# Kernel optimization log

Measured on AMD Instinct MI355X. Metric: run time of the kernel, lower is better.

The kernel has to match this reference:

```python
import jax, jax.numpy as jnp
import numpy as np

B, T, IN, H, L = 256, 80, 39, 256, 5


def _xavier(key, shape):
    fan_out, fan_in = shape[0], shape[1]
    std = (2.0 / (fan_in + fan_out)) ** 0.5
    return std * jax.random.normal(key, shape, dtype=jnp.float32)


def setup_inputs() -> dict:
    key = jax.random.key(0)
    ks = jax.random.split(key, 4 + 2 * L)
    x = jax.random.normal(ks[0], (B, T, IN), dtype=jnp.float32)
    # PyTorch LSTM params, gate order (i, f, g, o); biases zero per init.
    W_ih0 = _xavier(ks[1], (4 * H, IN))                       # layer 0 input weights
    W_ih_rest = jnp.stack([_xavier(ks[2 + l], (4 * H, H)) for l in range(L - 1)])  # [L-1,4H,H]
    W_hh = jnp.stack([_xavier(ks[1 + L + l], (4 * H, H)) for l in range(L)])       # [L,4H,H]
    b_ih = jnp.zeros((L, 4 * H), dtype=jnp.float32)
    b_hh = jnp.zeros((L, 4 * H), dtype=jnp.float32)
    fc_w = _xavier(ks[2 * L + 1], (1, H))
    fc_b = jnp.zeros((1,), dtype=jnp.float32)
    return {"x": x, "W_ih0": W_ih0, "W_ih_rest": W_ih_rest, "W_hh": W_hh,
            "b_ih": b_ih, "b_hh": b_hh, "fc_w": fc_w, "fc_b": fc_b}


def _lstm_layer(xs, W_ih, W_hh_l, b_ih_l, b_hh_l):
    # xs: [B,T,D]. Precompute input projection for all timesteps (one big GEMM).
    x_proj = jnp.einsum('btd,gd->btg', xs, W_ih) + b_ih_l + b_hh_l  # [B,T,4H]

    def step(carry, xp):
        h, c = carry
        gates = xp + h @ W_hh_l.T                 # [B,4H]
        i, f, g, o = jnp.split(gates, 4, axis=-1)
        c = jax.nn.sigmoid(f) * c + jax.nn.sigmoid(i) * jnp.tanh(g)
        h = jax.nn.sigmoid(o) * jnp.tanh(c)
        return (h, c), h

    b = xs.shape[0]
    h0 = jnp.zeros((b, H), dtype=xs.dtype)
    _, hs = jax.lax.scan(step, (h0, h0), jnp.swapaxes(x_proj, 0, 1))
    return jnp.swapaxes(hs, 0, 1)  # [B,T,H]


def reference(x, W_ih0, W_ih_rest, W_hh, b_ih, b_hh, fc_w, fc_b):
    h = _lstm_layer(x, W_ih0, W_hh[0], b_ih[0], b_hh[0])
    for l in range(1, L):
        h = _lstm_layer(h, W_ih_rest[l - 1], W_hh[l], b_ih[l], b_hh[l])
    out = jnp.einsum('bth,oh->bto', h, fc_w) + fc_b  # [B,T,1]
    return out[..., 0]  # [B,T]
```

## Files before the change

kernel.cpp:

```cpp
#include <hip/hip_runtime.h>

#define B_ 256
#define T_ 80
#define IN_ 39
#define H_ 256
#define G_ 1024
#define L_ 5
#define TC_ 16
#define NCH_ 5

#define XP_FLOATS   (B_ * TC_ * G_)
#define HBUF_FLOATS (B_ * T_ * H_)
#define CBUF_FLOATS (B_ * H_)
#define WG_FLOATS   (L_ * G_ * H_)
#define HX_FLOATS   (2 * 32 * 2048)
#define FLG_OFF_FLOATS (XP_FLOATS + HBUF_FLOATS + CBUF_FLOATS + WG_FLOATS + HX_FLOATS)

#define AG __HIP_MEMORY_SCOPE_AGENT

__device__ __forceinline__ float sigm(float x) { return 1.0f / (1.0f + expf(-x)); }
__device__ __forceinline__ void fma4(float4& a, float s, const float4& w) {
    a.x = fmaf(s, w.x, a.x); a.y = fmaf(s, w.y, a.y);
    a.z = fmaf(s, w.z, a.z); a.w = fmaf(s, w.w, a.w);
}
__device__ __forceinline__ void red4(float4& a) {
    a.x += __shfl_xor(a.x, 32); a.y += __shfl_xor(a.y, 32);
    a.z += __shfl_xor(a.z, 32); a.w += __shfl_xor(a.w, 32);
}
__device__ __forceinline__ float lo32(unsigned long long v) { return __uint_as_float((unsigned)v); }
__device__ __forceinline__ float hi32(unsigned long long v) { return __uint_as_float((unsigned)(v >> 32)); }

extern "C" __global__ void __launch_bounds__(256)
wt_kernel(const float* __restrict__ Whh, float* __restrict__ Wg) {
    const int gid = blockIdx.x * 256 + threadIdx.x;
    const int g4 = gid & 3;
    const int j  = (gid >> 2) & 31;
    const int k  = (gid >> 7) & 255;
    const int s  = (gid >> 15) & 7;
    const int l  = gid >> 18;
    Wg[gid] = Whh[((size_t)(l * 1024 + g4 * 256 + s * 32 + j)) * 256 + k];
}

extern "C" __global__ void __launch_bounds__(256)
proj_kernel(const float* __restrict__ src, const float* __restrict__ Wih,
            const float* __restrict__ bihl, const float* __restrict__ bhhl,
            float* __restrict__ xp, int K, int t0) {
    __shared__ float As[16 * 68];
    __shared__ float Bs[16 * 68];
    const int tid = threadIdx.x;
    const int mt = blockIdx.x >> 4, nt = blockIdx.x & 15;
    const int tx = tid & 15, ty = tid >> 4;
    const int lr = tid >> 2, lc4 = (tid & 3) << 2;

    const int ar = mt * 64 + lr;
    const int ab = ar >> 4;
    const int at = t0 + (ar & 15);
    const float* arow = src + ((size_t)ab * T_ + at) * K;
    const float* brow = Wih + (size_t)(nt * 64 + lr) * K;

    float acc[4][4];
    #pragma unroll
    for (int i = 0; i < 4; ++i)
        #pragma unroll
        for (int j = 0; j < 4; ++j) acc[i][j] = 0.0f;

    for (int k0 = 0; k0 < K; k0 += 16) {
        __syncthreads();
        if (K == IN_) {
            #pragma unroll
            for (int i = 0; i < 4; ++i) {
                int k = k0 + lc4 + i;
                As[(lc4 + i) * 68 + lr] = (k < IN_) ? arow[k] : 0.0f;
                Bs[(lc4 + i) * 68 + lr] = (k < IN_) ? brow[k] : 0.0f;
            }
        } else {
            float4 av = *(const float4*)(arow + k0 + lc4);
            float4 bv = *(const float4*)(brow + k0 + lc4);
            As[(lc4 + 0) * 68 + lr] = av.x;
            As[(lc4 + 1) * 68 + lr] = av.y;
            As[(lc4 + 2) * 68 + lr] = av.z;
            As[(lc4 + 3) * 68 + lr] = av.w;
            Bs[(lc4 + 0) * 68 + lr] = bv.x;
            Bs[(lc4 + 1) * 68 + lr] = bv.y;
            Bs[(lc4 + 2) * 68 + lr] = bv.z;
            Bs[(lc4 + 3) * 68 + lr] = bv.w;
        }
        __syncthreads();
        #pragma unroll
        for (int kk = 0; kk < 16; ++kk) {
            float4 a4 = *(const float4*)&As[kk * 68 + ty * 4];
            float4 b4 = *(const float4*)&Bs[kk * 68 + tx * 4];
            acc[0][0] += a4.x * b4.x; acc[0][1] += a4.x * b4.y;
            acc[0][2] += a4.x * b4.z; acc[0][3] += a4.x * b4.w;
            acc[1][0] += a4.y * b4.x; acc[1][1] += a4.y * b4.y;
            acc[1][2] += a4.y * b4.z; acc[1][3] += a4.y * b4.w;
            acc[2][0] += a4.z * b4.x; acc[2][1] += a4.z * b4.y;
            acc[2][2] += a4.z * b4.z; acc[2][3] += a4.z * b4.w;
            acc[3][0] += a4.w * b4.x; acc[3][1] += a4.w * b4.y;
            acc[3][2] += a4.w * b4.z; acc[3][3] += a4.w * b4.w;
        }
    }
    const int col = nt * 64 + tx * 4;
    const float bs0 = bihl[col + 0] + bhhl[col + 0];
    const float bs1 = bihl[col + 1] + bhhl[col + 1];
    const float bs2 = bihl[col + 2] + bhhl[col + 2];
    const float bs3 = bihl[col + 3] + bhhl[col + 3];
    #pragma unroll
    for (int i = 0; i < 4; ++i) {
        const int row = mt * 64 + ty * 4 + i;
        float4 o;
        o.x = acc[i][0] + bs0; o.y = acc[i][1] + bs1;
        o.z = acc[i][2] + bs2; o.w = acc[i][3] + bs3;
        *(float4*)&xp[(size_t)row * G_ + col] = o;
    }
}

extern "C" __global__ void __launch_bounds__(512, 2)
rec5_kernel(const float* __restrict__ xp, const float* __restrict__ Wg_l,
            float* __restrict__ hbuf, float* __restrict__ cbuf,
            float* __restrict__ hx, int* __restrict__ flg,
            int t0, int chkb, int first) {
    __shared__ float sH[2048];
    __shared__ float sP[8 * 32 * 36];

    const int tid = threadIdx.x;
    const int bid = blockIdx.x;
    const int grp = bid & 31;
    const int s   = bid >> 5;
    const int jj  = tid & 31;
    const int ks  = tid >> 5;
    const int w   = tid >> 6;
    const int fb  = (tid >> 5) & 7;
    const int fj  = tid & 31;
    const int bglob = grp * 8 + fb;
    const int unit  = s * 32 + fj;
    int* flg_g = flg + grp * 32;

    const float4* Wg4 = (const float4*)Wg_l + (size_t)s * 8192;
    float4 wreg[16];
    #pragma unroll
    for (int kk = 0; kk < 16; ++kk)
        wreg[kk] = Wg4[(size_t)(ks * 16 + kk) * 32 + jj];

    float creg = 0.0f;
    if (tid < 256 && !first) creg = cbuf[(size_t)bglob * H_ + unit];

    const float4* sH4 = (const float4*)sH;

    for (int tt = 0; tt < TC_; ++tt) {
        const int t = t0 + tt;

        float x0 = 0.f, x1 = 0.f, x2 = 0.f, x3 = 0.f;
        if (tid < 256) {
            const size_t xrow = ((size_t)bglob * TC_ + tt) * G_ + unit;
            x0 = xp[xrow];
            x1 = xp[xrow + 256];
            x2 = xp[xrow + 512];
            x3 = xp[xrow + 768];
        }

        if (tt == 0) {
            if (first) {
                for (int i = tid; i < 2048; i += 512) sH[i] = 0.0f;
            } else if (tid < 256) {
                const int u = tid;
                #pragma unroll
                for (int bb = 0; bb < 8; ++bb)
                    sH[u * 8 + bb] = hbuf[((size_t)(grp * 8 + bb) * T_ + (t0 - 1)) * H_ + u];
            }
        } else {
            if (tid < 8) {
                const int tgt = chkb + tt;
                while (__hip_atomic_load(flg_g + tid, __ATOMIC_RELAXED, AG) < tgt)
                    __builtin_amdgcn_s_sleep(1);
            }
            __syncthreads();
            if (tid < 256) {
                const unsigned long long* hs =
                    (const unsigned long long*)(hx + (size_t)(((tt - 1) & 1) * 32 + grp) * 2048);
                const int u = tid;
                unsigned long long v0 = __hip_atomic_load(hs + u * 4 + 0, __ATOMIC_RELAXED, AG);
                unsigned long long v1 = __hip_atomic_load(hs + u * 4 + 1, __ATOMIC_RELAXED, AG);
                unsigned long long v2 = __hip_atomic_load(hs + u * 4 + 2, __ATOMIC_RELAXED, AG);
                unsigned long long v3 = __hip_atomic_load(hs + u * 4 + 3, __ATOMIC_RELAXED, AG);
                float4 fa, fbv;
                fa.x = lo32(v0); fa.y = hi32(v0); fa.z = lo32(v1); fa.w = hi32(v1);
                fbv.x = lo32(v2); fbv.y = hi32(v2); fbv.z = lo32(v3); fbv.w = hi32(v3);
                *(float4*)&sH[u * 8] = fa;
                *(float4*)&sH[u * 8 + 4] = fbv;
            }
        }

        __syncthreads();

        float4 a0 = {0,0,0,0}, a1 = {0,0,0,0}, a2 = {0,0,0,0}, a3 = {0,0,0,0};
        float4 a4 = {0,0,0,0}, a5 = {0,0,0,0}, a6 = {0,0,0,0}, a7 = {0,0,0,0};
        #pragma unroll
        for (int kk = 0; kk < 16; ++kk) {
            const int k = ks * 16 + kk;
            const float4 wv = wreg[kk];
            const float4 ha = sH4[k * 2];
            const float4 hb = sH4[k * 2 + 1];
            fma4(a0, ha.x, wv); fma4(a1, ha.y, wv);
            fma4(a2, ha.z, wv); fma4(a3, ha.w, wv);
            fma4(a4, hb.x, wv); fma4(a5, hb.y, wv);
            fma4(a6, hb.z, wv); fma4(a7, hb.w, wv);
        }
        red4(a0); red4(a1); red4(a2); red4(a3);
        red4(a4); red4(a5); red4(a6); red4(a7);
        if ((tid & 63) < 32) {
            float4* pp = (float4*)&sP[(w * 32 + jj) * 36];
            pp[0] = a0; pp[1] = a1; pp[2] = a2; pp[3] = a3;
            pp[4] = a4; pp[5] = a5; pp[6] = a6; pp[7] = a7;
        }
        __syncthreads();

        if (tid < 256) {
            float4 g4;
            g4.x = x0; g4.y = x1; g4.z = x2; g4.w = x3;
            #pragma unroll
            for (int w2 = 0; w2 < 8; ++w2) {
                const float4 pw = *(const float4*)&sP[(w2 * 32 + fj) * 36 + fb * 4];
                g4.x += pw.x; g4.y += pw.y; g4.z += pw.z; g4.w += pw.w;
            }
            const float I = sigm(g4.x);
            const float F = sigm(g4.y);
            const float Gt = tanhf(g4.z);
            const float O = sigm(g4.w);
            creg = F * creg + I * Gt;
            const float hval = O * tanhf(creg);
            hbuf[((size_t)bglob * T_ + t) * H_ + unit] = hval;

            if (tt < TC_ - 1) {
                __hip_atomic_store(hx + (size_t)((tt & 1) * 32 + grp) * 2048 + unit * 8 + fb,
                                   hval, __ATOMIC_RELAXED, AG);
            }
        }

        if (tt < TC_ - 1) {
            asm volatile("s_waitcnt vmcnt(0)" ::: "memory");
            __syncthreads();
            if (tid == 0)
                __hip_atomic_store(flg_g + s, chkb + tt + 1, __ATOMIC_RELAXED, AG);
        }
    }

    if (tid < 256) cbuf[(size_t)bglob * H_ + unit] = creg;
}

extern "C" __global__ void __launch_bounds__(128)
fc_kernel(const float* __restrict__ hbuf, const float* __restrict__ fcw,
          const float* __restrict__ fcb, float* __restrict__ out) {
    __shared__ float wsm[256];
    const int tid = threadIdx.x;
    const int b = blockIdx.x;
    if (tid < 64) ((float4*)wsm)[tid] = ((const float4*)fcw)[tid];
    __syncthreads();
    if (tid < T_) {
        const float4* h4p = (const float4*)(hbuf + ((size_t)b * T_ + tid) * H_);
        const float4* w4p = (const float4*)wsm;
        float acc = fcb[0];
        #pragma unroll 8
        for (int k4 = 0; k4 < 64; ++k4) {
            float4 h4 = h4p[k4], w4 = w4p[k4];
            acc += h4.x * w4.x + h4.y * w4.y + h4.z * w4.z + h4.w * w4.w;
        }
        out[b * T_ + tid] = acc;
    }
}

extern "C" void kernel_launch(void* const* d_in, const int* in_sizes, int n_in,
                              void* d_out, int out_size, void* d_ws, size_t ws_size,
                              hipStream_t stream) {
    (void)in_sizes; (void)n_in; (void)out_size; (void)ws_size;
    const float* x    = (const float*)d_in[0];
    const float* Wih0 = (const float*)d_in[1];
    const float* Wihr = (const float*)d_in[2];
    const float* Whh  = (const float*)d_in[3];
    const float* bih  = (const float*)d_in[4];
    const float* bhh  = (const float*)d_in[5];
    const float* fcw  = (const float*)d_in[6];
    const float* fcb  = (const float*)d_in[7];
    float* out = (float*)d_out;
    float* ws  = (float*)d_ws;

    float* xp   = ws;
    float* hbuf = ws + XP_FLOATS;
    float* cbuf = hbuf + HBUF_FLOATS;
    float* wg   = cbuf + CBUF_FLOATS;
    float* hx   = wg + WG_FLOATS;
    int*   flg  = (int*)(ws + FLG_OFF_FLOATS);

    hipMemsetAsync(flg, 0, 32 * 32 * sizeof(int), stream);
    hipLaunchKernelGGL(wt_kernel, dim3(WG_FLOATS / 256), dim3(256), 0, stream, Whh, wg);

    for (int l = 0; l < L_; ++l) {
        const int K = (l == 0) ? IN_ : H_;
        const float* src = (l == 0) ? x : hbuf;
        const float* Wih = (l == 0) ? Wih0 : (Wihr + (size_t)(l - 1) * G_ * H_);
        const float* Wg_l = wg + (size_t)l * (G_ * H_);
        for (int ch = 0; ch < NCH_; ++ch) {
            const int t0 = ch * TC_;
            const int chkb = (l * NCH_ + ch) * (TC_ - 1);
            hipLaunchKernelGGL(proj_kernel, dim3(1024), dim3(256), 0, stream,
                               src, Wih, bih + l * G_, bhh + l * G_, xp, K, t0);
            hipLaunchKernelGGL(rec5_kernel, dim3(256), dim3(512), 0, stream,
                               xp, Wg_l, hbuf, cbuf, hx, flg, t0, chkb, ch == 0 ? 1 : 0);
        }
    }
    hipLaunchKernelGGL(fc_kernel, dim3(B_), dim3(128), 0, stream, hbuf, fcw, fcb, out);
}
```

Before: 2.582 ms.

## Overlap next-chunk input projection with current recurrence via helper blocks

Merges the per-chunk projection GEMM into the recurrent kernel. An extra 256 helper blocks compute the input projection for the next (layer, chunk) into a double-buffered xp, while the first 256 blocks run the current chunk's recurrence. Only the first projection is launched on its own, so the serial projection launch between recurrence chunks goes away and the GEMM hides behind the latency-bound recurrence. The cost is a second xp buffer and helper blocks sharing CUs with the spin-waiting recurrence blocks, which may slow the critical path.

```diff
diff --git a/kernel.cpp b/kernel.cpp
--- a/kernel.cpp
+++ b/kernel.cpp
@@ -14,7 +14,6 @@
 #define CBUF_FLOATS (B_ * H_)
 #define WG_FLOATS   (L_ * G_ * H_)
 #define HX_FLOATS   (2 * 32 * 2048)
-#define FLG_OFF_FLOATS (XP_FLOATS + HBUF_FLOATS + CBUF_FLOATS + WG_FLOATS + HX_FLOATS)
 
 #define AG __HIP_MEMORY_SCOPE_AGENT
 
@@ -116,136 +115,217 @@
 }
 
 extern "C" __global__ void __launch_bounds__(512, 2)
-rec5_kernel(const float* __restrict__ xp, const float* __restrict__ Wg_l,
-            float* __restrict__ hbuf, float* __restrict__ cbuf,
-            float* __restrict__ hx, int* __restrict__ flg,
-            int t0, int chkb, int first) {
-    __shared__ float sH[2048];
-    __shared__ float sP[8 * 32 * 36];
+fused_kernel(const float* __restrict__ xp, const float* __restrict__ Wg_l,
+             float* __restrict__ hbuf, float* __restrict__ cbuf,
+             float* __restrict__ hx, int* __restrict__ flg,
+             int t0, int chkb, int first,
+             int do_help, float* __restrict__ xpn, const float* __restrict__ hsrc,
+             const float* __restrict__ wih_n, const float* __restrict__ bih_n,
+             const float* __restrict__ bhh_n, int Kn, int t0n) {
+    __shared__ float smem[11264];
 
     const int tid = threadIdx.x;
     const int bid = blockIdx.x;
-    const int grp = bid & 31;
-    const int s   = bid >> 5;
-    const int jj  = tid & 31;
-    const int ks  = tid >> 5;
-    const int w   = tid >> 6;
-    const int fb  = (tid >> 5) & 7;
-    const int fj  = tid & 31;
-    const int bglob = grp * 8 + fb;
-    const int unit  = s * 32 + fj;
-    int* flg_g = flg + grp * 32;
-
-    const float4* Wg4 = (const float4*)Wg_l + (size_t)s * 8192;
-    float4 wreg[16];
-    #pragma unroll
-    for (int kk = 0; kk < 16; ++kk)
-        wreg[kk] = Wg4[(size_t)(ks * 16 + kk) * 32 + jj];
-
-    float creg = 0.0f;
-    if (tid < 256 && !first) creg = cbuf[(size_t)bglob * H_ + unit];
-
-    const float4* sH4 = (const float4*)sH;
-
-    for (int tt = 0; tt < TC_; ++tt) {
-        const int t = t0 + tt;
-
-        float x0 = 0.f, x1 = 0.f, x2 = 0.f, x3 = 0.f;
-        if (tid < 256) {
-            const size_t xrow = ((size_t)bglob * TC_ + tt) * G_ + unit;
-            x0 = xp[xrow];
-            x1 = xp[xrow + 256];
-            x2 = xp[xrow + 512];
-            x3 = xp[xrow + 768];
+
+    if (bid < 256) {
+        float* sH = smem;
+        float* sP = smem + 2048;
+        const int grp = bid & 31;
+        const int s   = bid >> 5;
+        const int jj  = tid & 31;
+        const int ks  = tid >> 5;
+        const int w   = tid >> 6;
+        const int fb  = (tid >> 5) & 7;
+        const int fj  = tid & 31;
+        const int bglob = grp * 8 + fb;
+        const int unit  = s * 32 + fj;
+        int* flg_g = flg + grp * 32;
+
+        const float4* Wg4 = (const float4*)Wg_l + (size_t)s * 8192;
+        float4 wreg[16];
+        #pragma unroll
+        for (int kk = 0; kk < 16; ++kk)
+            wreg[kk] = Wg4[(size_t)(ks * 16 + kk) * 32 + jj];
+
+        float creg = 0.0f;
+        if (tid < 256 && !first) creg = cbuf[(size_t)bglob * H_ + unit];
+
+        const float4* sH4 = (const float4*)sH;
+
+        for (int tt = 0; tt < TC_; ++tt) {
+            const int t = t0 + tt;
+
+            float x0 = 0.f, x1 = 0.f, x2 = 0.f, x3 = 0.f;
+            if (tid < 256) {
+                const size_t xrow = ((size_t)bglob * TC_ + tt) * G_ + unit;
+                x0 = xp[xrow];
+                x1 = xp[xrow + 256];
+                x2 = xp[xrow + 512];
+                x3 = xp[xrow + 768];
+            }
+
+            if (tt == 0) {
+                if (first) {
+                    for (int i = tid; i < 2048; i += 512) sH[i] = 0.0f;
+                } else if (tid < 256) {
+                    const int u = tid;
+                    #pragma unroll
+                    for (int bb = 0; bb < 8; ++bb)
+                        sH[u * 8 + bb] = hbuf[((size_t)(grp * 8 + bb) * T_ + (t0 - 1)) * H_ + u];
+                }
+            } else {
+                if (tid < 8) {
+                    const int tgt = chkb + tt;
+                    while (__hip_atomic_load(flg_g + tid, __ATOMIC_RELAXED, AG) < tgt)
+                        __builtin_amdgcn_s_sleep(1);
+                }
+                __syncthreads();
+                if (tid < 256) {
+                    const unsigned long long* hs =
+                        (const unsigned long long*)(hx + (size_t)(((tt - 1) & 1) * 32 + grp) * 2048);
+                    const int u = tid;
+                    unsigned long long v0 = __hip_atomic_load(hs + u * 4 + 0, __ATOMIC_RELAXED, AG);
+                    unsigned long long v1 = __hip_atomic_load(hs + u * 4 + 1, __ATOMIC_RELAXED, AG);
+                    unsigned long long v2 = __hip_atomic_load(hs + u * 4 + 2, __ATOMIC_RELAXED, AG);
+                    unsigned long long v3 = __hip_atomic_load(hs + u * 4 + 3, __ATOMIC_RELAXED, AG);
+                    float4 fa, fbv;
+                    fa.x = lo32(v0); fa.y = hi32(v0); fa.z = lo32(v1); fa.w = hi32(v1);
+                    fbv.x = lo32(v2); fbv.y = hi32(v2); fbv.z = lo32(v3); fbv.w = hi32(v3);
+                    *(float4*)&sH[u * 8] = fa;
+                    *(float4*)&sH[u * 8 + 4] = fbv;
+                }
+            }
+
+            __syncthreads();
+
+            float4 a0 = {0,0,0,0}, a1 = {0,0,0,0}, a2 = {0,0,0,0}, a3 = {0,0,0,0};
+            float4 a4 = {0,0,0,0}, a5 = {0,0,0,0}, a6 = {0,0,0,0}, a7 = {0,0,0,0};
+            #pragma unroll
+            for (int kk = 0; kk < 16; ++kk) {
+                const int k = ks * 16 + kk;
+                const float4 wv = wreg[kk];
+                const float4 ha = sH4[k * 2];
+                const float4 hb = sH4[k * 2 + 1];
+                fma4(a0, ha.x, wv); fma4(a1, ha.y, wv);
+                fma4(a2, ha.z, wv); fma4(a3, ha.w, wv);
+                fma4(a4, hb.x, wv); fma4(a5, hb.y, wv);
+                fma4(a6, hb.z, wv); fma4(a7, hb.w, wv);
+            }
+            red4(a0); red4(a1); red4(a2); red4(a3);
+            red4(a4); red4(a5); red4(a6); red4(a7);
+            if ((tid & 63) < 32) {
+                float4* pp = (float4*)&sP[(w * 32 + jj) * 36];
+                pp[0] = a0; pp[1] = a1; pp[2] = a2; pp[3] = a3;
+                pp[4] = a4; pp[5] = a5; pp[6] = a6; pp[7] = a7;
+            }
+            __syncthreads();
+
+            if (tid < 256) {
+                float4 g4;
+                g4.x = x0; g4.y = x1; g4.z = x2; g4.w = x3;
+                #pragma unroll
+                for (int w2 = 0; w2 < 8; ++w2) {
+                    const float4 pw = *(const float4*)&sP[(w2 * 32 + fj) * 36 + fb * 4];
+                    g4.x += pw.x; g4.y += pw.y; g4.z += pw.z; g4.w += pw.w;
+                }
+                const float I = sigm(g4.x);
+                const float F = sigm(g4.y);
+                const float Gt = tanhf(g4.z);
+                const float O = sigm(g4.w);
+                creg = F * creg + I * Gt;
+                const float hval = O * tanhf(creg);
+                hbuf[((size_t)bglob * T_ + t) * H_ + unit] = hval;
+                if (tt < TC_ - 1) {
+                    __hip_atomic_store(hx + (size_t)((tt & 1) * 32 + grp) * 2048 + unit * 8 + fb,
+                                       hval, __ATOMIC_RELAXED, AG);
+                }
+            }
+
+            if (tt < TC_ - 1) {
+                asm volatile("s_waitcnt vmcnt(0)" ::: "memory");
+                __syncthreads();
+                if (tid == 0)
+                    __hip_atomic_store(flg_g + s, chkb + tt + 1, __ATOMIC_RELAXED, AG);
+            }
         }
 
-        if (tt == 0) {
-            if (first) {
-                for (int i = tid; i < 2048; i += 512) sH[i] = 0.0f;
-            } else if (tid < 256) {
-                const int u = tid;
+        if (tid < 256) cbuf[(size_t)bglob * H_ + unit] = creg;
+    } else {
+        if (!do_help) return;
+        const int hb = bid - 256;
+        const int team = tid >> 8;
+        const int t2 = tid & 255;
+        float* As = smem + team * 2176;
+        float* Bs = As + 1088;
+        const int tx = t2 & 15, ty = t2 >> 4;
+        const int lr = t2 >> 2, lc4 = (t2 & 3) << 2;
+
+        for (int r = 0; r < 2; ++r) {
+            const int tile = hb * 4 + team * 2 + r;
+            const int mt = tile >> 4, nt = tile & 15;
+            const int ar = mt * 64 + lr;
+            const int ab = ar >> 4;
+            const int at = t0n + (ar & 15);
+            const float* arow = hsrc + ((size_t)ab * T_ + at) * Kn;
+            const float* brow = wih_n + (size_t)(nt * 64 + lr) * Kn;
+
+            float acc[4][4];
+            #pragma unroll
+            for (int i = 0; i < 4; ++i)
                 #pragma unroll
-                for (int bb = 0; bb < 8; ++bb)
-                    sH[u * 8 + bb] = hbuf[((size_t)(grp * 8 + bb) * T_ + (t0 - 1)) * H_ + u];
-            }
-        } else {
-            if (tid < 8) {
-                const int tgt = chkb + tt;
-                while (__hip_atomic_load(flg_g + tid, __ATOMIC_RELAXED, AG) < tgt)
-                    __builtin_amdgcn_s_sleep(1);
-            }
-            __syncthreads();
-            if (tid < 256) {
-                const unsigned long long* hs =
-                    (const unsigned long long*)(hx + (size_t)(((tt - 1) & 1) * 32 + grp) * 2048);
-                const int u = tid;
-                unsigned long long v0 = __hip_atomic_load(hs + u * 4 + 0, __ATOMIC_RELAXED, AG);
-                unsigned long long v1 = __hip_atomic_load(hs + u * 4 + 1, __ATOMIC_RELAXED, AG);
-                unsigned long long v2 = __hip_atomic_load(hs + u * 4 + 2, __ATOMIC_RELAXED, AG);
-                unsigned long long v3 = __hip_atomic_load(hs + u * 4 + 3, __ATOMIC_RELAXED, AG);
-                float4 fa, fbv;
-                fa.x = lo32(v0); fa.y = hi32(v0); fa.z = lo32(v1); fa.w = hi32(v1);
-                fbv.x = lo32(v2); fbv.y = hi32(v2); fbv.z = lo32(v3); fbv.w = hi32(v3);
-                *(float4*)&sH[u * 8] = fa;
-                *(float4*)&sH[u * 8 + 4] = fbv;
-            }
-        }
-
-        __syncthreads();
-
-        float4 a0 = {0,0,0,0}, a1 = {0,0,0,0}, a2 = {0,0,0,0}, a3 = {0,0,0,0};
-        float4 a4 = {0,0,0,0}, a5 = {0,0,0,0}, a6 = {0,0,0,0}, a7 = {0,0,0,0};
-        #pragma unroll
-        for (int kk = 0; kk < 16; ++kk) {
-            const int k = ks * 16 + kk;
-            const float4 wv = wreg[kk];
-            const float4 ha = sH4[k * 2];
-            const float4 hb = sH4[k * 2 + 1];
-            fma4(a0, ha.x, wv); fma4(a1, ha.y, wv);
-            fma4(a2, ha.z, wv); fma4(a3, ha.w, wv);
-            fma4(a4, hb.x, wv); fma4(a5, hb.y, wv);
-            fma4(a6, hb.z, wv); fma4(a7, hb.w, wv);
-        }
-        red4(a0); red4(a1); red4(a2); red4(a3);
-        red4(a4); red4(a5); red4(a6); red4(a7);
-        if ((tid & 63) < 32) {
-            float4* pp = (float4*)&sP[(w * 32 + jj) * 36];
-            pp[0] = a0; pp[1] = a1; pp[2] = a2; pp[3] = a3;
-            pp[4] = a4; pp[5] = a5; pp[6] = a6; pp[7] = a7;
-        }
-        __syncthreads();
-
-        if (tid < 256) {
-            float4 g4;
-            g4.x = x0; g4.y = x1; g4.z = x2; g4.w = x3;
+                for (int j = 0; j < 4; ++j) acc[i][j] = 0.0f;
+
+            for (int k0 = 0; k0 < Kn; k0 += 16) {
+                __syncthreads();
+                if (Kn == IN_) {
+                    #pragma unroll
+                    for (int i = 0; i < 4; ++i) {
+                        int k = k0 + lc4 + i;
+                        As[(lc4 + i) * 68 + lr] = (k < IN_) ? arow[k] : 0.0f;
+                        Bs[(lc4 + i) * 68 + lr] = (k < IN_) ? brow[k] : 0.0f;
+                    }
+                } else {
+                    float4 av = *(const float4*)(arow + k0 + lc4);
+                    float4 bv = *(const float4*)(brow + k0 + lc4);
+                    As[(lc4 + 0) * 68 + lr] = av.x;
+                    As[(lc4 + 1) * 68 + lr] = av.y;
+                    As[(lc4 + 2) * 68 + lr] = av.z;
+                    As[(lc4 + 3) * 68 + lr] = av.w;
+                    Bs[(lc4 + 0) * 68 + lr] = bv.x;
+                    Bs[(lc4 + 1) * 68 + lr] = bv.y;
+                    Bs[(lc4 + 2) * 68 + lr] = bv.z;
+                    Bs[(lc4 + 3) * 68 + lr] = bv.w;
+                }
+                __syncthreads();
+                #pragma unroll
+                for (int kk = 0; kk < 16; ++kk) {
+                    float4 a4 = *(const float4*)&As[kk * 68 + ty * 4];
+                    float4 b4 = *(const float4*)&Bs[kk * 68 + tx * 4];
+                    acc[0][0] += a4.x * b4.x; acc[0][1] += a4.x * b4.y;
+                    acc[0][2] += a4.x * b4.z; acc[0][3] += a4.x * b4.w;
+                    acc[1][0] += a4.y * b4.x; acc[1][1] += a4.y * b4.y;
+                    acc[1][2] += a4.y * b4.z; acc[1][3] += a4.y * b4.w;
+                    acc[2][0] += a4.z * b4.x; acc[2][1] += a4.z * b4.y;
+                    acc[2][2] += a4.z * b4.z; acc[2][3] += a4.z * b4.w;
+                    acc[3][0] += a4.w * b4.x; acc[3][1] += a4.w * b4.y;
+                    acc[3][2] += a4.w * b4.z; acc[3][3] += a4.w * b4.w;
+                }
+            }
+            const int col = nt * 64 + tx * 4;
+            const float bs0 = bih_n[col + 0] + bhh_n[col + 0];
+            const float bs1 = bih_n[col + 1] + bhh_n[col + 1];
+            const float bs2 = bih_n[col + 2] + bhh_n[col + 2];
+            const float bs3 = bih_n[col + 3] + bhh_n[col + 3];
             #pragma unroll
-            for (int w2 = 0; w2 < 8; ++w2) {
-                const float4 pw = *(const float4*)&sP[(w2 * 32 + fj) * 36 + fb * 4];
-                g4.x += pw.x; g4.y += pw.y; g4.z += pw.z; g4.w += pw.w;
-            }
-            const float I = sigm(g4.x);
-            const float F = sigm(g4.y);
-            const float Gt = tanhf(g4.z);
-            const float O = sigm(g4.w);
-            creg = F * creg + I * Gt;
-            const float hval = O * tanhf(creg);
-            hbuf[((size_t)bglob * T_ + t) * H_ + unit] = hval;
-
-            if (tt < TC_ - 1) {
-                __hip_atomic_store(hx + (size_t)((tt & 1) * 32 + grp) * 2048 + unit * 8 + fb,
-                                   hval, __ATOMIC_RELAXED, AG);
-            }
-        }
-
-        if (tt < TC_ - 1) {
-            asm volatile("s_waitcnt vmcnt(0)" ::: "memory");
-            __syncthreads();
-            if (tid == 0)
-                __hip_atomic_store(flg_g + s, chkb + tt + 1, __ATOMIC_RELAXED, AG);
+            for (int i = 0; i < 4; ++i) {
+                const int row = mt * 64 + ty * 4 + i;
+                float4 o;
+                o.x = acc[i][0] + bs0; o.y = acc[i][1] + bs1;
+                o.z = acc[i][2] + bs2; o.w = acc[i][3] + bs3;
+                *(float4*)&xpn[(size_t)row * G_ + col] = o;
+            }
         }
     }
-
-    if (tid < 256) cbuf[(size_t)bglob * H_ + unit] = creg;
 }
 
 extern "C" __global__ void __launch_bounds__(128)
@@ -284,29 +364,40 @@
     float* out = (float*)d_out;
     float* ws  = (float*)d_ws;
 
-    float* xp   = ws;
-    float* hbuf = ws + XP_FLOATS;
+    float* xp0  = ws;
+    float* xp1  = ws + XP_FLOATS;
+    float* hbuf = ws + 2 * XP_FLOATS;
     float* cbuf = hbuf + HBUF_FLOATS;
     float* wg   = cbuf + CBUF_FLOATS;
     float* hx   = wg + WG_FLOATS;
-    int*   flg  = (int*)(ws + FLG_OFF_FLOATS);
+    int*   flg  = (int*)(hx + HX_FLOATS);
 
     hipMemsetAsync(flg, 0, 32 * 32 * sizeof(int), stream);
     hipLaunchKernelGGL(wt_kernel, dim3(WG_FLOATS / 256), dim3(256), 0, stream, Whh, wg);
-
-    for (int l = 0; l < L_; ++l) {
-        const int K = (l == 0) ? IN_ : H_;
-        const float* src = (l == 0) ? x : hbuf;
-        const float* Wih = (l == 0) ? Wih0 : (Wihr + (size_t)(l - 1) * G_ * H_);
+    hipLaunchKernelGGL(proj_kernel, dim3(1024), dim3(256), 0, stream,
+                       x, Wih0, bih, bhh, xp0, IN_, 0);
+
+    for (int q = 0; q < L_ * NCH_; ++q) {
+        const int l = q / NCH_, ch = q % NCH_;
+        float* xpc = (q & 1) ? xp1 : xp0;
         const float* Wg_l = wg + (size_t)l * (G_ * H_);
-        for (int ch = 0; ch < NCH_; ++ch) {
-            const int t0 = ch * TC_;
-            const int chkb = (l * NCH_ + ch) * (TC_ - 1);
-            hipLaunchKernelGGL(proj_kernel, dim3(1024), dim3(256), 0, stream,
-                               src, Wih, bih + l * G_, bhh + l * G_, xp, K, t0);
-            hipLaunchKernelGGL(rec5_kernel, dim3(256), dim3(512), 0, stream,
-                               xp, Wg_l, hbuf, cbuf, hx, flg, t0, chkb, ch == 0 ? 1 : 0);
-        }
+        const int t0 = ch * TC_;
+        const int chkb = q * (TC_ - 1);
+        const int first = (ch == 0) ? 1 : 0;
+
+        const int do_help = (q < L_ * NCH_ - 1) ? 1 : 0;
+        const int q2 = do_help ? (q + 1) : 1;
+        const int l2 = q2 / NCH_, c2 = q2 % NCH_;
+        float* xpn = ((q + 1) & 1) ? xp1 : xp0;
+        const float* hsrc = (l2 == 0) ? x : hbuf;
+        const float* wn   = (l2 == 0) ? Wih0 : (Wihr + (size_t)(l2 - 1) * G_ * H_);
+        const int Kn  = (l2 == 0) ? IN_ : H_;
+        const int t0n = c2 * TC_;
+
+        hipLaunchKernelGGL(fused_kernel, dim3(512), dim3(512), 0, stream,
+                           xpc, Wg_l, hbuf, cbuf, hx, flg, t0, chkb, first,
+                           do_help, xpn, hsrc, wn, bih + l2 * G_, bhh + l2 * G_,
+                           Kn, t0n);
     }
     hipLaunchKernelGGL(fc_kernel, dim3(B_), dim3(128), 0, stream, hbuf, fcw, fcb, out);
 }
```

Result: no change. 2.612 ms (+1.2%).

## Interleave gate projections per unit and vectorize cross-block hidden-state loads

Applied to the files above, without the earlier changes.

The projection kernel now writes its output with the four gates of each hidden unit interleaved, so the recurrent kernel reads its four gate inputs with a single float4 load instead of four strided scalar loads. The exchange of hidden state between blocks swaps four 64-bit relaxed atomic loads for two inline-asm dwordx4 loads with sc0 sc1 cache-bypass bits, which cuts the instruction count on the latency-critical per-step path. In exchange, the projection stores become scattered scalar writes, and the coherence of the exchange now rests on the cache-policy bits in hand-written assembly rather than on atomics.

```diff
diff --git a/kernel.cpp b/kernel.cpp
--- a/kernel.cpp
+++ b/kernel.cpp
@@ -27,8 +27,13 @@
     a.x += __shfl_xor(a.x, 32); a.y += __shfl_xor(a.y, 32);
     a.z += __shfl_xor(a.z, 32); a.w += __shfl_xor(a.w, 32);
 }
-__device__ __forceinline__ float lo32(unsigned long long v) { return __uint_as_float((unsigned)v); }
-__device__ __forceinline__ float hi32(unsigned long long v) { return __uint_as_float((unsigned)(v >> 32)); }
+
+__device__ __forceinline__ void ld_mall_32B(const float* p, float4& a, float4& b) {
+    asm volatile("global_load_dwordx4 %0, %2, off sc0 sc1\n\t"
+                 "global_load_dwordx4 %1, %2, off offset:16 sc0 sc1\n\t"
+                 "s_waitcnt vmcnt(0)"
+                 : "=&v"(a), "=&v"(b) : "v"(p) : "memory");
+}
 
 extern "C" __global__ void __launch_bounds__(256)
 wt_kernel(const float* __restrict__ Whh, float* __restrict__ Wg) {
@@ -101,6 +106,8 @@
         }
     }
     const int col = nt * 64 + tx * 4;
+    const int g  = col >> 8;
+    const int u0 = col & 255;
     const float bs0 = bihl[col + 0] + bhhl[col + 0];
     const float bs1 = bihl[col + 1] + bhhl[col + 1];
     const float bs2 = bihl[col + 2] + bhhl[col + 2];
@@ -108,15 +115,16 @@
     #pragma unroll
     for (int i = 0; i < 4; ++i) {
         const int row = mt * 64 + ty * 4 + i;
-        float4 o;
-        o.x = acc[i][0] + bs0; o.y = acc[i][1] + bs1;
-        o.z = acc[i][2] + bs2; o.w = acc[i][3] + bs3;
-        *(float4*)&xp[(size_t)row * G_ + col] = o;
+        float* xr = xp + (size_t)row * G_;
+        xr[(u0 + 0) * 4 + g] = acc[i][0] + bs0;
+        xr[(u0 + 1) * 4 + g] = acc[i][1] + bs1;
+        xr[(u0 + 2) * 4 + g] = acc[i][2] + bs2;
+        xr[(u0 + 3) * 4 + g] = acc[i][3] + bs3;
     }
 }
 
 extern "C" __global__ void __launch_bounds__(512, 2)
-rec5_kernel(const float* __restrict__ xp, const float* __restrict__ Wg_l,
+rec7_kernel(const float* __restrict__ xp, const float* __restrict__ Wg_l,
             float* __restrict__ hbuf, float* __restrict__ cbuf,
             float* __restrict__ hx, int* __restrict__ flg,
             int t0, int chkb, int first) {
@@ -152,11 +160,8 @@
 
         float x0 = 0.f, x1 = 0.f, x2 = 0.f, x3 = 0.f;
         if (tid < 256) {
-            const size_t xrow = ((size_t)bglob * TC_ + tt) * G_ + unit;
-            x0 = xp[xrow];
-            x1 = xp[xrow + 256];
-            x2 = xp[xrow + 512];
-            x3 = xp[xrow + 768];
+            const float4 xv = *(const float4*)&xp[((size_t)bglob * TC_ + tt) * G_ + unit * 4];
+            x0 = xv.x; x1 = xv.y; x2 = xv.z; x3 = xv.w;
         }
 
         if (tt == 0) {
@@ -176,18 +181,12 @@
             }
             __syncthreads();
             if (tid < 256) {
-                const unsigned long long* hs =
-                    (const unsigned long long*)(hx + (size_t)(((tt - 1) & 1) * 32 + grp) * 2048);
-                const int u = tid;
-                unsigned long long v0 = __hip_atomic_load(hs + u * 4 + 0, __ATOMIC_RELAXED, AG);
-                unsigned long long v1 = __hip_atomic_load(hs + u * 4 + 1, __ATOMIC_RELAXED, AG);
-                unsigned long long v2 = __hip_atomic_load(hs + u * 4 + 2, __ATOMIC_RELAXED, AG);
-                unsigned long long v3 = __hip_atomic_load(hs + u * 4 + 3, __ATOMIC_RELAXED, AG);
+                const float* hsf = hx + (size_t)(((tt - 1) & 1) * 32 + grp) * 2048
+                                      + (size_t)tid * 8;
                 float4 fa, fbv;
-                fa.x = lo32(v0); fa.y = hi32(v0); fa.z = lo32(v1); fa.w = hi32(v1);
-                fbv.x = lo32(v2); fbv.y = hi32(v2); fbv.z = lo32(v3); fbv.w = hi32(v3);
-                *(float4*)&sH[u * 8] = fa;
-                *(float4*)&sH[u * 8 + 4] = fbv;
+                ld_mall_32B(hsf, fa, fbv);
+                *(float4*)&sH[tid * 8] = fa;
+                *(float4*)&sH[tid * 8 + 4] = fbv;
             }
         }
 
@@ -304,7 +303,7 @@
             const int chkb = (l * NCH_ + ch) * (TC_ - 1);
             hipLaunchKernelGGL(proj_kernel, dim3(1024), dim3(256), 0, stream,
                                src, Wih, bih + l * G_, bhh + l * G_, xp, K, t0);
-            hipLaunchKernelGGL(rec5_kernel, dim3(256), dim3(512), 0, stream,
+            hipLaunchKernelGGL(rec7_kernel, dim3(256), dim3(512), 0, stream,
                                xp, Wg_l, hbuf, cbuf, hx, flg, t0, chkb, ch == 0 ? 1 : 0);
         }
     }
```

New measurement: 2.947 ms. 1.14x slower.
